# Kernel optimization log

Hardware: AMD Instinct MI355X
Metric: run time of the kernel (lower is better)

## Reference

```python
import jax, jax.numpy as jnp
import numpy as np
from jax import lax

B, C, H, W = 8, 256, 64, 64
E, K, OUT = 9, 3, 256
EPS = 1e-5


def setup_inputs() -> dict:
    key = jax.random.key(0)
    ks = jax.random.split(key, 12)
    return {
        "x": jax.random.normal(ks[0], (B, C, H, W), jnp.float32),
        "w_experts": jax.random.normal(ks[1], (E, C, K, K), jnp.float32) * 0.1,  # depthwise kernels (O=C, I=1 folded)
        "bn_gamma": jax.random.normal(ks[2], (E, C), jnp.float32) * 0.1 + 1.0,
        "bn_beta": jax.random.normal(ks[3], (E, C), jnp.float32) * 0.1,
        "bn_mean": jax.random.normal(ks[4], (E, C), jnp.float32) * 0.1,
        "bn_var": jax.random.uniform(ks[5], (E, C), jnp.float32, 0.5, 1.5),
        "scales": jnp.full((E, C), 0.1, jnp.float32),
        "w_out": jax.random.normal(ks[6], (OUT, C), jnp.float32) * (1.0 / np.sqrt(C)),  # 1x1 conv weight
        "out_gamma": jax.random.normal(ks[7], (OUT,), jnp.float32) * 0.1 + 1.0,
        "out_beta": jax.random.normal(ks[8], (OUT,), jnp.float32) * 0.1,
        "out_mean": jax.random.normal(ks[9], (OUT,), jnp.float32) * 0.1,
        "out_var": jax.random.uniform(ks[10], (OUT,), jnp.float32, 0.5, 1.5),
    }


def reference(x, w_experts, bn_gamma, bn_beta, bn_mean, bn_var, scales,
              w_out, out_gamma, out_beta, out_mean, out_var):
    # All E depthwise convs in ONE grouped conv: groups=C, E outputs per group.
    # kernel (E,C,K,K) -> (C,E,K,K) -> (C*E, 1, K, K); output group c holds experts of channel c.
    k = jnp.transpose(w_experts, (1, 0, 2, 3)).reshape(C * E, 1, K, K)
    y = lax.conv_general_dilated(
        x, k, window_strides=(1, 1), padding="SAME",
        feature_group_count=C,
        dimension_numbers=("NCHW", "OIHW", "NCHW"),
    )  # [B, C*E, H, W]
    y = y.reshape(x.shape[0], C, E, H, W)

    # Fold BN (eval-mode, running stats) and per-expert channel scale, then sum over experts.
    t = bn_gamma * lax.rsqrt(bn_var + EPS)          # [E, C]
    eff_scale = t * scales                          # [E, C]
    eff_bias = ((bn_beta - bn_mean * t) * scales).sum(0)  # [C]
    moe = jnp.einsum("bcehw,ec->bchw", y, eff_scale) + eff_bias[None, :, None, None]
    moe = jax.nn.silu(moe)

    # out_prj: 1x1 conv + BN + SiLU
    out = jnp.einsum("bchw,oc->bohw", moe, w_out)
    t2 = out_gamma * lax.rsqrt(out_var + EPS)       # [OUT]
    out = out * t2[None, :, None, None] + (out_beta - out_mean * t2)[None, :, None, None]
    return jax.nn.silu(out)
```

## Files before the change

### kernel.cpp

```cpp
#include <hip/hip_runtime.h>

#define EPS 1e-5f

typedef __attribute__((ext_vector_type(8))) __bf16 bf16x8;
typedef __attribute__((ext_vector_type(4))) float f32x4;

__device__ __forceinline__ void async_copy16(const void* g, void* l) {
  __builtin_amdgcn_global_load_lds(
      (const __attribute__((address_space(1))) unsigned int*)g,
      (__attribute__((address_space(3))) unsigned int*)l, 16, 0, 0);
}

__device__ __forceinline__ float silu_f(float v) {
  return v / (1.f + __expf(-v));
}

__global__ __launch_bounds__(256) void prep_kernel(
    const float* __restrict__ w_experts, const float* __restrict__ bn_gamma,
    const float* __restrict__ bn_beta, const float* __restrict__ bn_mean,
    const float* __restrict__ bn_var, const float* __restrict__ scales,
    const float* __restrict__ w_out, const float* __restrict__ out_gamma,
    const float* __restrict__ out_beta, const float* __restrict__ out_mean,
    const float* __restrict__ out_var,
    float* __restrict__ eff_kernel, float* __restrict__ eff_bias,
    __bf16* __restrict__ w_eff, float* __restrict__ bias2)
{
  const int t = threadIdx.x;
  if (blockIdx.x == 0) {
    const int c = t;
    float k9[9];
#pragma unroll
    for (int r = 0; r < 9; ++r) k9[r] = 0.f;
    float bias = 0.f;
    for (int e = 0; e < 9; ++e) {
      const int ec = e * 256 + c;
      const float tt = bn_gamma[ec] * rsqrtf(bn_var[ec] + EPS);
      const float sc = scales[ec];
      const float es = tt * sc;
      bias += (bn_beta[ec] - bn_mean[ec] * tt) * sc;
      const float* wp = w_experts + (size_t)ec * 9;
#pragma unroll
      for (int r = 0; r < 9; ++r) k9[r] += es * wp[r];
    }
#pragma unroll
    for (int r = 0; r < 9; ++r) eff_kernel[c * 9 + r] = k9[r];
    eff_bias[c] = bias;
    const float t2 = out_gamma[c] * rsqrtf(out_var[c] + EPS);
    bias2[c] = out_beta[c] - out_mean[c] * t2;
  } else {
    const int i = (blockIdx.x - 1) * 256 + t;
    const int o = i >> 8;
    const float t2 = out_gamma[o] * rsqrtf(out_var[o] + EPS);
    w_eff[i] = (__bf16)(w_out[i] * t2);
  }
}

__global__ __launch_bounds__(256) void dw_kernel(
    const float* __restrict__ x, const float* __restrict__ eff_kernel,
    const float* __restrict__ eff_bias, __bf16* __restrict__ moe)
{
  __shared__ __align__(16) __bf16 lds_t[64 * 72];
  __shared__ float kern_s[64 * 9];
  __shared__ float bias_s[64];
  const int t = threadIdx.x;
  const int cg = blockIdx.x & 3;
  const int h = (blockIdx.x >> 2) & 63;
  const int b = blockIdx.x >> 8;

  if (t < 64) bias_s[t] = eff_bias[cg * 64 + t];
  for (int i = t; i < 576; i += 256) kern_s[i] = eff_kernel[cg * 576 + i];
  __syncthreads();

  const int lane = t & 63;
  const int wv = t >> 6;
  const int lg = lane >> 4;
  const int wq = lane & 15;
  const int w4 = wq * 4;
  const bool up_ok = (h > 0), dn_ok = (h < 63);

#pragma unroll
  for (int cc4 = 0; cc4 < 4; ++cc4) {
    const int ch = wv * 16 + cc4 * 4 + lg;
    const float* xc = x + ((size_t)(b * 256 + cg * 64 + ch) * 64) * 64;

    float4 v0, v1, v2;
    v1 = *(const float4*)(xc + h * 64 + w4);
    if (up_ok) v0 = *(const float4*)(xc + (h - 1) * 64 + w4);
    else       v0 = make_float4(0.f, 0.f, 0.f, 0.f);
    if (dn_ok) v2 = *(const float4*)(xc + (h + 1) * 64 + w4);
    else       v2 = make_float4(0.f, 0.f, 0.f, 0.f);

    float k[9];
#pragma unroll
    for (int j = 0; j < 9; ++j) k[j] = kern_s[ch * 9 + j];
    const float bias = bias_s[ch];

    float rowv[3][6];
    const float4 vv[3] = {v0, v1, v2};
#pragma unroll
    for (int r = 0; r < 3; ++r) {
      float vl = __shfl_up(vv[r].w, 1);
      float vr = __shfl_down(vv[r].x, 1);
      rowv[r][0] = (wq == 0) ? 0.f : vl;
      rowv[r][1] = vv[r].x;
      rowv[r][2] = vv[r].y;
      rowv[r][3] = vv[r].z;
      rowv[r][4] = vv[r].w;
      rowv[r][5] = (wq == 15) ? 0.f : vr;
    }

#pragma unroll
    for (int j = 0; j < 4; ++j) {
      float s = bias;
#pragma unroll
      for (int r = 0; r < 3; ++r)
        s += k[r * 3] * rowv[r][j] + k[r * 3 + 1] * rowv[r][j + 1] + k[r * 3 + 2] * rowv[r][j + 2];
      lds_t[(w4 + j) * 72 + ch] = (__bf16)silu_f(s);
    }
  }
  __syncthreads();

  const int pix0 = (b * 64 + h) * 64;
#pragma unroll
  for (int it = 0; it < 2; ++it) {
    const int idx = it * 256 + t;
    const int w2 = idx >> 3;
    const int c8 = (idx & 7) * 8;
    const uint4 v = *(const uint4*)&lds_t[w2 * 72 + c8];
    *(uint4*)&moe[(size_t)(pix0 + w2) * 256 + cg * 64 + c8] = v;
  }
}

__global__ __launch_bounds__(256) void gemm_kernel(
    const __bf16* __restrict__ moe, const __bf16* __restrict__ w_eff,
    const float* __restrict__ bias2, float* __restrict__ out)
{
  __shared__ __align__(16) __bf16 A_lds[256 * 64];
  __shared__ __align__(16) __bf16 B_lds[32 * 64];
  const int t = threadIdx.x;
  const int lane = t & 63;
  const int wv = t >> 6;
  const int P0 = blockIdx.x * 32;
  const int quad = lane >> 4, l15 = lane & 15;
  const int wave_o = wv * 64;

  f32x4 acc[4][2];
#pragma unroll
  for (int i = 0; i < 4; ++i)
#pragma unroll
    for (int j = 0; j < 2; ++j) acc[i][j] = (f32x4){0.f, 0.f, 0.f, 0.f};

  const char* gA0 = (const char*)w_eff;
  const char* gB0 = (const char*)moe + (size_t)P0 * 512;

  for (int kt = 0; kt < 4; ++kt) {
#pragma unroll
    for (int i = 0; i < 8; ++i) {
      const int lin = i * 4096 + t * 16;
      const int r = lin >> 7;
      const int kb = lin & 127;
      async_copy16(gA0 + (size_t)r * 512 + kt * 128 + kb, (char*)A_lds + lin);
    }
    {
      const int r = t >> 3;
      const int kb = (t & 7) * 16;
      async_copy16(gB0 + (size_t)r * 512 + kt * 128 + kb, (char*)B_lds + t * 16);
    }
    __syncthreads();
#pragma unroll
    for (int kk = 0; kk < 2; ++kk) {
      bf16x8 af[4], bf[2];
#pragma unroll
      for (int i = 0; i < 4; ++i)
        af[i] = *(const bf16x8*)&A_lds[(wave_o + i * 16 + l15) * 64 + kk * 32 + quad * 8];
#pragma unroll
      for (int j = 0; j < 2; ++j)
        bf[j] = *(const bf16x8*)&B_lds[(j * 16 + l15) * 64 + kk * 32 + quad * 8];
#pragma unroll
      for (int i = 0; i < 4; ++i)
#pragma unroll
        for (int j = 0; j < 2; ++j)
          acc[i][j] = __builtin_amdgcn_mfma_f32_16x16x32_bf16(af[i], bf[j], acc[i][j], 0, 0, 0);
    }
    __syncthreads();
  }

  const int b = P0 >> 12;
  const int p_in_b = P0 & 4095;
  float* outb = out + (size_t)b * 256 * 4096;
#pragma unroll
  for (int i = 0; i < 4; ++i) {
#pragma unroll
    for (int r = 0; r < 4; ++r) {
      const int o = wave_o + i * 16 + quad * 4 + r;
      const float bo = bias2[o];
#pragma unroll
      for (int j = 0; j < 2; ++j) {
        const int p = p_in_b + j * 16 + l15;
        outb[(size_t)o * 4096 + p] = silu_f(acc[i][j][r] + bo);
      }
    }
  }
}

extern "C" void kernel_launch(void* const* d_in, const int* in_sizes, int n_in,
                              void* d_out, int out_size, void* d_ws, size_t ws_size,
                              hipStream_t stream) {
  const float* x         = (const float*)d_in[0];
  const float* w_experts = (const float*)d_in[1];
  const float* bn_gamma  = (const float*)d_in[2];
  const float* bn_beta   = (const float*)d_in[3];
  const float* bn_mean   = (const float*)d_in[4];
  const float* bn_var    = (const float*)d_in[5];
  const float* scales    = (const float*)d_in[6];
  const float* w_out     = (const float*)d_in[7];
  const float* out_gamma = (const float*)d_in[8];
  const float* out_beta  = (const float*)d_in[9];
  const float* out_mean  = (const float*)d_in[10];
  const float* out_var   = (const float*)d_in[11];
  float* out = (float*)d_out;

  char* ws = (char*)d_ws;
  __bf16* moe       = (__bf16*)(ws);
  float* eff_kernel = (float*)(ws + 16777216);
  float* eff_bias   = (float*)(ws + 16786432);
  __bf16* w_eff     = (__bf16*)(ws + 16787456);
  float* bias2      = (float*)(ws + 16918528);

  hipLaunchKernelGGL(prep_kernel, dim3(257), dim3(256), 0, stream,
                     w_experts, bn_gamma, bn_beta, bn_mean, bn_var, scales,
                     w_out, out_gamma, out_beta, out_mean, out_var,
                     eff_kernel, eff_bias, w_eff, bias2);
  hipLaunchKernelGGL(dw_kernel, dim3(2048), dim3(256), 0, stream,
                     x, eff_kernel, eff_bias, moe);
  hipLaunchKernelGGL(gemm_kernel, dim3(1024), dim3(256), 0, stream,
                     moe, w_eff, bias2, out);
}
```

Before: 128.1 us.

## Fuse depthwise MoE conv and 1x1 projection GEMM into one kernel

Merges the depthwise expert conv kernel and the bf16 MFMA 1x1-conv GEMM into one kernel. Each block computes one image row (64 pixels, all 256 channels) into LDS, then multiplies it by the folded output weights, read straight from global/L2 rather than staged in LDS. This removes the 16 MB bf16 intermediate write and reread plus one launch. In exchange there are fewer blocks (512), a larger LDS footprint, and weight fragments loaded per wave from global memory. Blocks are ordered so that neighbouring rows share halo rows in cache.

```diff
diff --git a/kernel.cpp b/kernel.cpp
--- a/kernel.cpp
+++ b/kernel.cpp
@@ -4,12 +4,6 @@
 
 typedef __attribute__((ext_vector_type(8))) __bf16 bf16x8;
 typedef __attribute__((ext_vector_type(4))) float f32x4;
-
-__device__ __forceinline__ void async_copy16(const void* g, void* l) {
-  __builtin_amdgcn_global_load_lds(
-      (const __attribute__((address_space(1))) unsigned int*)g,
-      (__attribute__((address_space(3))) unsigned int*)l, 16, 0, 0);
-}
 
 __device__ __forceinline__ float silu_f(float v) {
   return v / (1.f + __expf(-v));
@@ -55,20 +49,23 @@
   }
 }
 
-__global__ __launch_bounds__(256) void dw_kernel(
+__global__ __launch_bounds__(256) void fused_kernel(
     const float* __restrict__ x, const float* __restrict__ eff_kernel,
-    const float* __restrict__ eff_bias, __bf16* __restrict__ moe)
+    const float* __restrict__ eff_bias, const __bf16* __restrict__ w_eff,
+    const float* __restrict__ bias2, float* __restrict__ out)
 {
-  __shared__ __align__(16) __bf16 lds_t[64 * 72];
-  __shared__ float kern_s[64 * 9];
-  __shared__ float bias_s[64];
+  __shared__ __align__(16) __bf16 B_lds[64 * 264];
+  __shared__ float kern_s[256 * 9];
+  __shared__ float bias_s[256];
   const int t = threadIdx.x;
-  const int cg = blockIdx.x & 3;
-  const int h = (blockIdx.x >> 2) & 63;
-  const int b = blockIdx.x >> 8;
+  const int id = blockIdx.x;
+  const int hg = id & 7;
+  const int idx2 = id >> 3;
+  const int b = idx2 & 7;
+  const int h = hg * 8 + (idx2 >> 3);
 
-  if (t < 64) bias_s[t] = eff_bias[cg * 64 + t];
-  for (int i = t; i < 576; i += 256) kern_s[i] = eff_kernel[cg * 576 + i];
+  for (int i = t; i < 2304; i += 256) kern_s[i] = eff_kernel[i];
+  bias_s[t] = eff_bias[t];
   __syncthreads();
 
   const int lane = t & 63;
@@ -78,116 +75,77 @@
   const int w4 = wq * 4;
   const bool up_ok = (h > 0), dn_ok = (h < 63);
 
+  for (int cg = 0; cg < 4; ++cg) {
 #pragma unroll
-  for (int cc4 = 0; cc4 < 4; ++cc4) {
-    const int ch = wv * 16 + cc4 * 4 + lg;
-    const float* xc = x + ((size_t)(b * 256 + cg * 64 + ch) * 64) * 64;
+    for (int cc4 = 0; cc4 < 4; ++cc4) {
+      const int ch = cg * 64 + wv * 16 + cc4 * 4 + lg;
+      const float* xc = x + (size_t)(b * 256 + ch) * 4096;
 
-    float4 v0, v1, v2;
-    v1 = *(const float4*)(xc + h * 64 + w4);
-    if (up_ok) v0 = *(const float4*)(xc + (h - 1) * 64 + w4);
-    else       v0 = make_float4(0.f, 0.f, 0.f, 0.f);
-    if (dn_ok) v2 = *(const float4*)(xc + (h + 1) * 64 + w4);
-    else       v2 = make_float4(0.f, 0.f, 0.f, 0.f);
+      float4 v0, v1, v2;
+      v1 = *(const float4*)(xc + h * 64 + w4);
+      if (up_ok) v0 = *(const float4*)(xc + (h - 1) * 64 + w4);
+      else       v0 = make_float4(0.f, 0.f, 0.f, 0.f);
+      if (dn_ok) v2 = *(const float4*)(xc + (h + 1) * 64 + w4);
+      else       v2 = make_float4(0.f, 0.f, 0.f, 0.f);
 
-    float k[9];
+      float k[9];
 #pragma unroll
-    for (int j = 0; j < 9; ++j) k[j] = kern_s[ch * 9 + j];
-    const float bias = bias_s[ch];
+      for (int j = 0; j < 9; ++j) k[j] = kern_s[ch * 9 + j];
+      const float bias = bias_s[ch];
 
-    float rowv[3][6];
-    const float4 vv[3] = {v0, v1, v2};
+      float rowv[3][6];
+      const float4 vv[3] = {v0, v1, v2};
 #pragma unroll
-    for (int r = 0; r < 3; ++r) {
-      float vl = __shfl_up(vv[r].w, 1);
-      float vr = __shfl_down(vv[r].x, 1);
-      rowv[r][0] = (wq == 0) ? 0.f : vl;
-      rowv[r][1] = vv[r].x;
-      rowv[r][2] = vv[r].y;
-      rowv[r][3] = vv[r].z;
-      rowv[r][4] = vv[r].w;
-      rowv[r][5] = (wq == 15) ? 0.f : vr;
-    }
+      for (int r = 0; r < 3; ++r) {
+        float vl = __shfl_up(vv[r].w, 1);
+        float vr = __shfl_down(vv[r].x, 1);
+        rowv[r][0] = (wq == 0) ? 0.f : vl;
+        rowv[r][1] = vv[r].x;
+        rowv[r][2] = vv[r].y;
+        rowv[r][3] = vv[r].z;
+        rowv[r][4] = vv[r].w;
+        rowv[r][5] = (wq == 15) ? 0.f : vr;
+      }
 
 #pragma unroll
-    for (int j = 0; j < 4; ++j) {
-      float s = bias;
+      for (int j = 0; j < 4; ++j) {
+        float s = bias;
 #pragma unroll
-      for (int r = 0; r < 3; ++r)
-        s += k[r * 3] * rowv[r][j] + k[r * 3 + 1] * rowv[r][j + 1] + k[r * 3 + 2] * rowv[r][j + 2];
-      lds_t[(w4 + j) * 72 + ch] = (__bf16)silu_f(s);
+        for (int r = 0; r < 3; ++r)
+          s += k[r * 3] * rowv[r][j] + k[r * 3 + 1] * rowv[r][j + 1] + k[r * 3 + 2] * rowv[r][j + 2];
+        B_lds[(w4 + j) * 264 + ch] = (__bf16)silu_f(s);
+      }
     }
   }
   __syncthreads();
 
-  const int pix0 = (b * 64 + h) * 64;
-#pragma unroll
-  for (int it = 0; it < 2; ++it) {
-    const int idx = it * 256 + t;
-    const int w2 = idx >> 3;
-    const int c8 = (idx & 7) * 8;
-    const uint4 v = *(const uint4*)&lds_t[w2 * 72 + c8];
-    *(uint4*)&moe[(size_t)(pix0 + w2) * 256 + cg * 64 + c8] = v;
-  }
-}
-
-__global__ __launch_bounds__(256) void gemm_kernel(
-    const __bf16* __restrict__ moe, const __bf16* __restrict__ w_eff,
-    const float* __restrict__ bias2, float* __restrict__ out)
-{
-  __shared__ __align__(16) __bf16 A_lds[256 * 64];
-  __shared__ __align__(16) __bf16 B_lds[32 * 64];
-  const int t = threadIdx.x;
-  const int lane = t & 63;
-  const int wv = t >> 6;
-  const int P0 = blockIdx.x * 32;
-  const int quad = lane >> 4, l15 = lane & 15;
+  const int quad = lg;
+  const int l15 = wq;
   const int wave_o = wv * 64;
 
-  f32x4 acc[4][2];
+  f32x4 acc[4][4];
 #pragma unroll
   for (int i = 0; i < 4; ++i)
 #pragma unroll
-    for (int j = 0; j < 2; ++j) acc[i][j] = (f32x4){0.f, 0.f, 0.f, 0.f};
+    for (int j = 0; j < 4; ++j) acc[i][j] = (f32x4){0.f, 0.f, 0.f, 0.f};
 
-  const char* gA0 = (const char*)w_eff;
-  const char* gB0 = (const char*)moe + (size_t)P0 * 512;
-
-  for (int kt = 0; kt < 4; ++kt) {
 #pragma unroll
-    for (int i = 0; i < 8; ++i) {
-      const int lin = i * 4096 + t * 16;
-      const int r = lin >> 7;
-      const int kb = lin & 127;
-      async_copy16(gA0 + (size_t)r * 512 + kt * 128 + kb, (char*)A_lds + lin);
-    }
-    {
-      const int r = t >> 3;
-      const int kb = (t & 7) * 16;
-      async_copy16(gB0 + (size_t)r * 512 + kt * 128 + kb, (char*)B_lds + t * 16);
-    }
-    __syncthreads();
+  for (int kk = 0; kk < 8; ++kk) {
+    bf16x8 af[4], bf[4];
 #pragma unroll
-    for (int kk = 0; kk < 2; ++kk) {
-      bf16x8 af[4], bf[2];
+    for (int i = 0; i < 4; ++i)
+      af[i] = *(const bf16x8*)&w_eff[(size_t)(wave_o + i * 16 + l15) * 256 + kk * 32 + quad * 8];
 #pragma unroll
-      for (int i = 0; i < 4; ++i)
-        af[i] = *(const bf16x8*)&A_lds[(wave_o + i * 16 + l15) * 64 + kk * 32 + quad * 8];
+    for (int j = 0; j < 4; ++j)
+      bf[j] = *(const bf16x8*)&B_lds[(j * 16 + l15) * 264 + kk * 32 + quad * 8];
 #pragma unroll
-      for (int j = 0; j < 2; ++j)
-        bf[j] = *(const bf16x8*)&B_lds[(j * 16 + l15) * 64 + kk * 32 + quad * 8];
+    for (int i = 0; i < 4; ++i)
 #pragma unroll
-      for (int i = 0; i < 4; ++i)
-#pragma unroll
-        for (int j = 0; j < 2; ++j)
-          acc[i][j] = __builtin_amdgcn_mfma_f32_16x16x32_bf16(af[i], bf[j], acc[i][j], 0, 0, 0);
-    }
-    __syncthreads();
+      for (int j = 0; j < 4; ++j)
+        acc[i][j] = __builtin_amdgcn_mfma_f32_16x16x32_bf16(af[i], bf[j], acc[i][j], 0, 0, 0);
   }
 
-  const int b = P0 >> 12;
-  const int p_in_b = P0 & 4095;
-  float* outb = out + (size_t)b * 256 * 4096;
+  float* outb = out + (size_t)b * 256 * 4096 + h * 64;
 #pragma unroll
   for (int i = 0; i < 4; ++i) {
 #pragma unroll
@@ -195,8 +153,8 @@
       const int o = wave_o + i * 16 + quad * 4 + r;
       const float bo = bias2[o];
 #pragma unroll
-      for (int j = 0; j < 2; ++j) {
-        const int p = p_in_b + j * 16 + l15;
+      for (int j = 0; j < 4; ++j) {
+        const int p = j * 16 + l15;
         outb[(size_t)o * 4096 + p] = silu_f(acc[i][j][r] + bo);
       }
     }
@@ -221,18 +179,15 @@
   float* out = (float*)d_out;
 
   char* ws = (char*)d_ws;
-  __bf16* moe       = (__bf16*)(ws);
-  float* eff_kernel = (float*)(ws + 16777216);
-  float* eff_bias   = (float*)(ws + 16786432);
-  __bf16* w_eff     = (__bf16*)(ws + 16787456);
-  float* bias2      = (float*)(ws + 16918528);
+  float* eff_kernel = (float*)(ws);
+  float* eff_bias   = (float*)(ws + 9216);
+  __bf16* w_eff     = (__bf16*)(ws + 10240);
+  float* bias2      = (float*)(ws + 141312);
 
   hipLaunchKernelGGL(prep_kernel, dim3(257), dim3(256), 0, stream,
                      w_experts, bn_gamma, bn_beta, bn_mean, bn_var, scales,
                      w_out, out_gamma, out_beta, out_mean, out_var,
                      eff_kernel, eff_bias, w_eff, bias2);
-  hipLaunchKernelGGL(dw_kernel, dim3(2048), dim3(256), 0, stream,
-                     x, eff_kernel, eff_bias, moe);
-  hipLaunchKernelGGL(gemm_kernel, dim3(1024), dim3(256), 0, stream,
-                     moe, w_eff, bias2, out);
+  hipLaunchKernelGGL(fused_kernel, dim3(512), dim3(256), 0, stream,
+                     x, eff_kernel, eff_bias, w_eff, bias2, out);
 }
```

Result: no change. 126.2 us (-1.5%).
